# Kernel optimization log

Measured on AMD Instinct MI355X. Metric: run time of the kernel, lower is better.

## Reference

```python
import jax, jax.numpy as jnp
import numpy as np

D_MODEL = 1024
NUM_HEADS = 16
D_K = D_MODEL // NUM_HEADS
B, T = 2, 2048


def setup_inputs() -> dict:
    key = jax.random.key(0)
    ks = jax.random.split(key, 9)
    s = 1.0 / np.sqrt(D_MODEL)
    inp = {"x": jax.random.normal(ks[0], (B, T, D_MODEL), dtype=jnp.float32)}
    for i, name in enumerate(["q", "k", "v", "out"]):
        inp[f"W_{name}"] = jax.random.uniform(ks[1 + 2 * i], (D_MODEL, D_MODEL), jnp.float32, -s, s)
        inp[f"b_{name}"] = jax.random.uniform(ks[2 + 2 * i], (D_MODEL,), jnp.float32, -s, s)
    return inp


def reference(x, W_q, b_q, W_k, b_k, W_v, b_v, W_out, b_out):
    b, t, _ = x.shape
    # torch Linear: y = x @ W.T + b
    def proj(inp, W, bias):
        y = inp @ W.T + bias
        return y.reshape(b, -1, NUM_HEADS, D_K).transpose(0, 2, 1, 3)  # [B,H,T,d_k]

    Q = proj(x, W_q, b_q)
    K = proj(x, W_k, b_k)
    V = proj(x, W_v, b_v)
    scores = jnp.einsum("bhqd,bhkd->bhqk", Q, K) / jnp.sqrt(jnp.float32(D_K))
    attn = jax.nn.softmax(scores, axis=-1)
    ctx = jnp.einsum("bhqk,bhkd->bhqd", attn, V)
    ctx = ctx.transpose(0, 2, 1, 3).reshape(b, t, D_MODEL)
    return ctx @ W_out.T + b_out
```

## Files before the change

### kernel.cpp

```cpp
#include <hip/hip_runtime.h>
#include <hip/hip_bf16.h>

typedef __attribute__((ext_vector_type(8))) short short8;
typedef __attribute__((ext_vector_type(4))) short short4v;
typedef __attribute__((ext_vector_type(4))) float floatx4;

__device__ __forceinline__ unsigned short f2b(float f) {
  unsigned int v;
  __builtin_memcpy(&v, &f, 4);
  unsigned int r = (v + 0x7FFFu + ((v >> 16) & 1u)) >> 16;
  return (unsigned short)r;
}

__device__ __forceinline__ unsigned int f2b_pk(float a, float b) {
#if __has_builtin(__builtin_amdgcn_cvt_pk_bf16_f32)
  typedef __attribute__((ext_vector_type(2))) __bf16 bf16x2;
  bf16x2 r = __builtin_amdgcn_cvt_pk_bf16_f32(a, b);
  unsigned int u;
  __builtin_memcpy(&u, &r, 4);
  return u;
#else
  return ((unsigned int)f2b(b) << 16) | (unsigned int)f2b(a);
#endif
}

__device__ __forceinline__ float fast_exp2(float x) {
#if __has_builtin(__builtin_amdgcn_exp2f)
  return __builtin_amdgcn_exp2f(x);
#else
  return __builtin_exp2f(x);
#endif
}

__device__ __forceinline__ void async_copy16(const void* g, void* l) {
  __builtin_amdgcn_global_load_lds(
      (const __attribute__((address_space(1))) unsigned int*)g,
      (__attribute__((address_space(3))) unsigned int*)l, 16, 0, 0);
}

#define QSCALE 0.18033688011112042f


__global__ __launch_bounds__(256) void cvt_all_kernel(
    const float* __restrict__ x,
    const float* __restrict__ w0, const float* __restrict__ w1,
    const float* __restrict__ w2, const float* __restrict__ w3,
    unsigned short* __restrict__ xb,
    unsigned short* __restrict__ d0, unsigned short* __restrict__ d1,
    unsigned short* __restrict__ d2, unsigned short* __restrict__ d3)
{
  int gid = blockIdx.x * 256 + threadIdx.x;
  const float* src;
  unsigned short* dst;
  size_t off;
  if (gid < (1 << 20)) {
    src = x; dst = xb; off = gid;
  } else {
    int g = gid - (1 << 20);
    int w = g >> 18;
    off = g & 0x3FFFF;
    src = (w == 0) ? w0 : (w == 1) ? w1 : (w == 2) ? w2 : w3;
    dst = (w == 0) ? d0 : (w == 1) ? d1 : (w == 2) ? d2 : d3;
  }
  floatx4 v = *(const floatx4*)(src + off * 4);
  unsigned int lo = f2b_pk(v[0], v[1]), hi = f2b_pk(v[2], v[3]);
  unsigned long long r = ((unsigned long long)hi << 32) | lo;
  *(unsigned long long*)(dst + off * 4) = r;
}

__global__ __launch_bounds__(256) void gemm_qkv_kernel(
    const unsigned short* __restrict__ A,
    const unsigned short* __restrict__ W0, const unsigned short* __restrict__ W1,
    const unsigned short* __restrict__ W2,
    const float* __restrict__ bias0, const float* __restrict__ bias1,
    const float* __restrict__ bias2,
    unsigned short* __restrict__ Qo, unsigned short* __restrict__ Ko,
    unsigned short* __restrict__ VTo)
{
  const int z = blockIdx.z;
  const unsigned short* W  = (z == 0) ? W0 : (z == 1) ? W1 : W2;
  const float* bias        = (z == 0) ? bias0 : (z == 1) ? bias1 : bias2;

  __shared__ alignas(16) unsigned short sA[128 * 32];
  __shared__ alignas(16) unsigned short sB[128 * 32];

  const int tid  = threadIdx.x;
  const int lane = tid & 63;
  const int wave = tid >> 6;
  const int col  = lane & 15;
  const int quad = lane >> 4;
  const int wm   = (wave >> 1) * 64;
  const int wn   = (wave & 1) * 64;
  const int m0   = blockIdx.y * 128;
  const int n0   = blockIdx.x * 128;
  const int swz8 = (quad ^ ((col >> 1) & 3)) * 8;

  floatx4 acc[4][4];
#pragma unroll
  for (int i = 0; i < 4; ++i)
#pragma unroll
    for (int j = 0; j < 4; ++j) acc[i][j] = (floatx4){0.f, 0.f, 0.f, 0.f};

  for (int k0 = 0; k0 < 1024; k0 += 32) {
    __syncthreads();
#pragma unroll
    for (int i = 0; i < 2; ++i) {
      int c   = i * 256 + tid;
      int row = c >> 2;
      int cs  = (c & 3) ^ ((c >> 3) & 3);
      int ko  = cs * 8;
      async_copy16(A + (size_t)(m0 + row) * 1024 + k0 + ko, sA + c * 8);
      async_copy16(W + (size_t)(n0 + row) * 1024 + k0 + ko, sB + c * 8);
    }
    __syncthreads();
    short8 af[4], bf[4];
#pragma unroll
    for (int mi = 0; mi < 4; ++mi)
      af[mi] = *(const short8*)(sA + (wm + mi * 16 + col) * 32 + swz8);
#pragma unroll
    for (int ni = 0; ni < 4; ++ni)
      bf[ni] = *(const short8*)(sB + (wn + ni * 16 + col) * 32 + swz8);
#pragma unroll
    for (int mi = 0; mi < 4; ++mi)
#pragma unroll
      for (int ni = 0; ni < 4; ++ni)
        acc[mi][ni] = __builtin_amdgcn_mfma_f32_16x16x32_bf16(af[mi], bf[ni], acc[mi][ni], 0, 0, 0);
  }

#pragma unroll
  for (int ni = 0; ni < 4; ++ni) {
    int n = n0 + wn + ni * 16 + col;
    float bv = bias[n];
#pragma unroll
    for (int mi = 0; mi < 4; ++mi) {
      int mbase = m0 + wm + mi * 16 + quad * 4;
#pragma unroll
      for (int r = 0; r < 4; ++r) {
        int m = mbase + r;
        float val = acc[mi][ni][r] + bv;
        if (z == 0) {
          Qo[(size_t)m * 1024 + n] = f2b(val * QSCALE);
        } else if (z == 1) {
          Ko[(size_t)m * 1024 + n] = f2b(val);
        } else {
          int d = n & 63, h = n >> 6;
          int bb = m >> 11, t = m & 2047;
          VTo[(((size_t)bb * 16 + h) * 64 + d) * 2048 + t] = f2b(val);
        }
      }
    }
  }
}

__global__ __launch_bounds__(256) void gemm_out_kernel(
    const unsigned short* __restrict__ A, const unsigned short* __restrict__ W,
    const float* __restrict__ bias, float* __restrict__ DF)
{
  __shared__ alignas(16) unsigned short sA[128 * 32];
  __shared__ alignas(16) unsigned short sB[64 * 32];

  const int tid  = threadIdx.x;
  const int lane = tid & 63;
  const int wave = tid >> 6;
  const int col  = lane & 15;
  const int quad = lane >> 4;
  const int wm   = (wave >> 1) * 64;
  const int wn   = (wave & 1) * 32;
  const int m0   = blockIdx.y * 128;
  const int n0   = blockIdx.x * 64;
  const int swz8 = (quad ^ ((col >> 1) & 3)) * 8;

  floatx4 acc[4][2];
#pragma unroll
  for (int i = 0; i < 4; ++i)
#pragma unroll
    for (int j = 0; j < 2; ++j) acc[i][j] = (floatx4){0.f, 0.f, 0.f, 0.f};

  for (int k0 = 0; k0 < 1024; k0 += 32) {
    __syncthreads();
#pragma unroll
    for (int i = 0; i < 2; ++i) {
      int c   = i * 256 + tid;
      int row = c >> 2;
      int cs  = (c & 3) ^ ((c >> 3) & 3);
      async_copy16(A + (size_t)(m0 + row) * 1024 + k0 + cs * 8, sA + c * 8);
    }
    {
      int row = tid >> 2;
      int cs  = (tid & 3) ^ ((tid >> 3) & 3);
      async_copy16(W + (size_t)(n0 + row) * 1024 + k0 + cs * 8, sB + tid * 8);
    }
    __syncthreads();
    short8 af[4], bf[2];
#pragma unroll
    for (int mi = 0; mi < 4; ++mi)
      af[mi] = *(const short8*)(sA + (wm + mi * 16 + col) * 32 + swz8);
#pragma unroll
    for (int ni = 0; ni < 2; ++ni)
      bf[ni] = *(const short8*)(sB + (wn + ni * 16 + col) * 32 + swz8);
#pragma unroll
    for (int mi = 0; mi < 4; ++mi)
#pragma unroll
      for (int ni = 0; ni < 2; ++ni)
        acc[mi][ni] = __builtin_amdgcn_mfma_f32_16x16x32_bf16(af[mi], bf[ni], acc[mi][ni], 0, 0, 0);
  }

#pragma unroll
  for (int ni = 0; ni < 2; ++ni) {
    int n = n0 + wn + ni * 16 + col;
    float bv = bias[n];
#pragma unroll
    for (int mi = 0; mi < 4; ++mi) {
      int mbase = m0 + wm + mi * 16 + quad * 4;
#pragma unroll
      for (int r = 0; r < 4; ++r)
        DF[(size_t)(mbase + r) * 1024 + n] = acc[mi][ni][r] + bv;
    }
  }
}

__global__ __launch_bounds__(256, 6) void attention_kernel(
    const unsigned short* __restrict__ Q, const unsigned short* __restrict__ K,
    const unsigned short* __restrict__ VT, unsigned short* __restrict__ CTX)
{
  __shared__ alignas(16) unsigned short sQ[2 * 64 * 32];
  __shared__ alignas(16) unsigned short sK[2 * 64 * 32];
  __shared__ alignas(16) unsigned short sV[2 * 64 * 32];

  const int bh = blockIdx.x;
  const int b = bh >> 4, h = bh & 15;
  const int q0 = blockIdx.y * 64;
  const int tid  = threadIdx.x;
  const int lane = tid & 63;
  const int wave = tid >> 6;
  const int col  = lane & 15;
  const int quad = lane >> 4;
  const int swz8 = (quad ^ ((col >> 1) & 3)) * 8;

  const int srow = tid >> 2;
  const int sko  = ((tid & 3) ^ ((tid >> 3) & 3)) * 8;

#pragma unroll
  for (int i = 0; i < 2; ++i) {
    async_copy16(Q + (size_t)(b * 2048 + q0 + srow) * 1024 + h * 64 + i * 32 + sko,
                 sQ + (i * 256 + tid) * 8);
  }
  __syncthreads();
  short8 qf[2];
  qf[0] = *(const short8*)(sQ + (wave * 16 + col) * 32 + swz8);
  qf[1] = *(const short8*)(sQ + 2048 + (wave * 16 + col) * 32 + swz8);

  const int vsw  = (col >> 1) & 3;
  const int vch0 = ((quad >> 1) ^ vsw) * 8 + (quad & 1) * 4;
  const int vch1 = (((quad >> 1) | 2) ^ vsw) * 8 + (quad & 1) * 4;

  floatx4 Oacc[4];
#pragma unroll
  for (int nd = 0; nd < 4; ++nd) Oacc[nd] = (floatx4){0.f, 0.f, 0.f, 0.f};
  float lacc = 0.f;

  for (int kt = 0; kt < 2048; kt += 64) {
    __syncthreads();
#pragma unroll
    for (int i = 0; i < 2; ++i) {
      async_copy16(K + (size_t)(b * 2048 + kt + srow) * 1024 + h * 64 + i * 32 + sko,
                   sK + (i * 256 + tid) * 8);
      async_copy16(VT + ((size_t)bh * 64 + srow) * 2048 + kt + i * 32 + sko,
                   sV + (i * 256 + tid) * 8);
    }
    __syncthreads();

    floatx4 ST[4];
#pragma unroll
    for (int f = 0; f < 4; ++f) {
      ST[f] = (floatx4){0.f, 0.f, 0.f, 0.f};
      short8 kf0 = *(const short8*)(sK + (f * 16 + col) * 32 + swz8);
      ST[f] = __builtin_amdgcn_mfma_f32_16x16x32_bf16(kf0, qf[0], ST[f], 0, 0, 0);
      short8 kf1 = *(const short8*)(sK + 2048 + (f * 16 + col) * 32 + swz8);
      ST[f] = __builtin_amdgcn_mfma_f32_16x16x32_bf16(kf1, qf[1], ST[f], 0, 0, 0);
    }

    short8 pf[2];
#pragma unroll
    for (int s = 0; s < 2; ++s) {
      float p00 = fast_exp2(ST[2 * s][0]);
      float p01 = fast_exp2(ST[2 * s][1]);
      float p02 = fast_exp2(ST[2 * s][2]);
      float p03 = fast_exp2(ST[2 * s][3]);
      float p10 = fast_exp2(ST[2 * s + 1][0]);
      float p11 = fast_exp2(ST[2 * s + 1][1]);
      float p12 = fast_exp2(ST[2 * s + 1][2]);
      float p13 = fast_exp2(ST[2 * s + 1][3]);
      lacc += ((p00 + p01) + (p02 + p03)) + ((p10 + p11) + (p12 + p13));
      alignas(16) unsigned int d4[4] = {
          f2b_pk(p00, p01), f2b_pk(p02, p03), f2b_pk(p10, p11), f2b_pk(p12, p13)};
      __builtin_memcpy(&pf[s], d4, 16);
    }

#pragma unroll
    for (int s = 0; s < 2; ++s) {
#pragma unroll
      for (int nd = 0; nd < 4; ++nd) {
        const unsigned short* vrow = sV + s * 2048 + (nd * 16 + col) * 32;
        short4v v0 = *(const short4v*)(vrow + vch0);
        short4v v1 = *(const short4v*)(vrow + vch1);
        short8 vf = (short8){v0[0], v0[1], v0[2], v0[3], v1[0], v1[1], v1[2], v1[3]};
        Oacc[nd] = __builtin_amdgcn_mfma_f32_16x16x32_bf16(vf, pf[s], Oacc[nd], 0, 0, 0);
      }
    }
  }

  lacc += __shfl_xor(lacc, 16, 64);
  lacc += __shfl_xor(lacc, 32, 64);
  float inv = 1.f / lacc;

  {
    int q = q0 + wave * 16 + col;
    unsigned short* dst = CTX + (size_t)(b * 2048 + q) * 1024 + h * 64;
#pragma unroll
    for (int nd = 0; nd < 4; ++nd) {
      unsigned int lo = f2b_pk(Oacc[nd][0] * inv, Oacc[nd][1] * inv);
      unsigned int hi = f2b_pk(Oacc[nd][2] * inv, Oacc[nd][3] * inv);
      unsigned long long w = ((unsigned long long)hi << 32) | lo;
      *(unsigned long long*)(dst + nd * 16 + quad * 4) = w;
    }
  }
}

extern "C" void kernel_launch(void* const* d_in, const int* in_sizes, int n_in,
                              void* d_out, int out_size, void* d_ws, size_t ws_size,
                              hipStream_t stream) {
  const float* x   = (const float*)d_in[0];
  const float* W_q = (const float*)d_in[1];
  const float* b_q = (const float*)d_in[2];
  const float* W_k = (const float*)d_in[3];
  const float* b_k = (const float*)d_in[4];
  const float* W_v = (const float*)d_in[5];
  const float* b_v = (const float*)d_in[6];
  const float* W_o = (const float*)d_in[7];
  const float* b_o = (const float*)d_in[8];
  float* out = (float*)d_out;

  const size_t NX = (size_t)4096 * 1024;
  const size_t NW = (size_t)1024 * 1024;

  unsigned short* p   = (unsigned short*)d_ws;
  unsigned short* xb  = p;  p += NX;
  unsigned short* Wqb = p;  p += NW;
  unsigned short* Wkb = p;  p += NW;
  unsigned short* Wvb = p;  p += NW;
  unsigned short* Wob = p;  p += NW;
  unsigned short* Q   = p;  p += NX;
  unsigned short* Kb  = p;  p += NX;
  unsigned short* VT  = p;  p += NX;
  unsigned short* CTX = p;  p += NX;

  dim3 blk(256);
  cvt_all_kernel<<<dim3(8192), blk, 0, stream>>>(
      x, W_q, W_k, W_v, W_o, xb, Wqb, Wkb, Wvb, Wob);
  gemm_qkv_kernel<<<dim3(8, 32, 3), blk, 0, stream>>>(
      xb, Wqb, Wkb, Wvb, b_q, b_k, b_v, Q, Kb, VT);
  attention_kernel<<<dim3(32, 32), blk, 0, stream>>>(Q, Kb, VT, CTX);
  gemm_out_kernel<<<dim3(16, 32), blk, 0, stream>>>(CTX, Wob, b_o, out);
}
```

Before: 204.9 us.

## Pre-permute V^T layout in projection and compute softmax row sums via MFMA

The V projection epilogue now writes V^T with tokens permuted within each 32-wide chunk, packing four bf16 values into one 64-bit store. This lets the attention kernel load each V fragment with a single 16-byte LDS read instead of two 8-byte reads plus a shuffle. The softmax denominator is now accumulated with an extra MFMA against a ones vector instead of per-lane adds and cross-lane shuffles. The row sum is then built from bf16-rounded probabilities, which slightly changes numerics.

```diff
diff --git a/kernel.cpp b/kernel.cpp
--- a/kernel.cpp
+++ b/kernel.cpp
@@ -2,7 +2,6 @@
 #include <hip/hip_bf16.h>
 
 typedef __attribute__((ext_vector_type(8))) short short8;
-typedef __attribute__((ext_vector_type(4))) short short4v;
 typedef __attribute__((ext_vector_type(4))) float floatx4;
 
 __device__ __forceinline__ unsigned short f2b(float f) {
@@ -134,18 +133,22 @@
 #pragma unroll
     for (int mi = 0; mi < 4; ++mi) {
       int mbase = m0 + wm + mi * 16 + quad * 4;
-#pragma unroll
-      for (int r = 0; r < 4; ++r) {
-        int m = mbase + r;
-        float val = acc[mi][ni][r] + bv;
-        if (z == 0) {
-          Qo[(size_t)m * 1024 + n] = f2b(val * QSCALE);
-        } else if (z == 1) {
-          Ko[(size_t)m * 1024 + n] = f2b(val);
-        } else {
-          int d = n & 63, h = n >> 6;
-          int bb = m >> 11, t = m & 2047;
-          VTo[(((size_t)bb * 16 + h) * 64 + d) * 2048 + t] = f2b(val);
+      if (z == 2) {
+        int d = n & 63, hh = n >> 6;
+        int bb = mbase >> 11, tb = mbase & 2047;
+        int tl = tb & 31, tbase = tb & ~31;
+        int pp = ((tl & 15) >> 2) * 8 + ((tl >> 4) & 1) * 4;
+        unsigned int lo = f2b_pk(acc[mi][ni][0] + bv, acc[mi][ni][1] + bv);
+        unsigned int hi = f2b_pk(acc[mi][ni][2] + bv, acc[mi][ni][3] + bv);
+        unsigned long long w = ((unsigned long long)hi << 32) | lo;
+        *(unsigned long long*)(VTo + (((size_t)bb * 16 + hh) * 64 + d) * 2048 + tbase + pp) = w;
+      } else {
+#pragma unroll
+        for (int r = 0; r < 4; ++r) {
+          int m = mbase + r;
+          float val = acc[mi][ni][r] + bv;
+          if (z == 0) Qo[(size_t)m * 1024 + n] = f2b(val * QSCALE);
+          else        Ko[(size_t)m * 1024 + n] = f2b(val);
         }
       }
     }
@@ -250,14 +253,18 @@
   qf[0] = *(const short8*)(sQ + (wave * 16 + col) * 32 + swz8);
   qf[1] = *(const short8*)(sQ + 2048 + (wave * 16 + col) * 32 + swz8);
 
-  const int vsw  = (col >> 1) & 3;
-  const int vch0 = ((quad >> 1) ^ vsw) * 8 + (quad & 1) * 4;
-  const int vch1 = (((quad >> 1) | 2) ^ vsw) * 8 + (quad & 1) * 4;
+  short8 ones;
+  {
+    unsigned short o = 0x3F80;
+    short tmp[8] = {(short)o, (short)o, (short)o, (short)o,
+                    (short)o, (short)o, (short)o, (short)o};
+    __builtin_memcpy(&ones, tmp, 16);
+  }
 
   floatx4 Oacc[4];
 #pragma unroll
   for (int nd = 0; nd < 4; ++nd) Oacc[nd] = (floatx4){0.f, 0.f, 0.f, 0.f};
-  float lacc = 0.f;
+  floatx4 Osum = (floatx4){0.f, 0.f, 0.f, 0.f};
 
   for (int kt = 0; kt < 2048; kt += 64) {
     __syncthreads();
@@ -291,7 +298,6 @@
       float p11 = fast_exp2(ST[2 * s + 1][1]);
       float p12 = fast_exp2(ST[2 * s + 1][2]);
       float p13 = fast_exp2(ST[2 * s + 1][3]);
-      lacc += ((p00 + p01) + (p02 + p03)) + ((p10 + p11) + (p12 + p13));
       alignas(16) unsigned int d4[4] = {
           f2b_pk(p00, p01), f2b_pk(p02, p03), f2b_pk(p10, p11), f2b_pk(p12, p13)};
       __builtin_memcpy(&pf[s], d4, 16);
@@ -299,20 +305,16 @@
 
 #pragma unroll
     for (int s = 0; s < 2; ++s) {
+      Osum = __builtin_amdgcn_mfma_f32_16x16x32_bf16(ones, pf[s], Osum, 0, 0, 0);
 #pragma unroll
       for (int nd = 0; nd < 4; ++nd) {
-        const unsigned short* vrow = sV + s * 2048 + (nd * 16 + col) * 32;
-        short4v v0 = *(const short4v*)(vrow + vch0);
-        short4v v1 = *(const short4v*)(vrow + vch1);
-        short8 vf = (short8){v0[0], v0[1], v0[2], v0[3], v1[0], v1[1], v1[2], v1[3]};
+        short8 vf = *(const short8*)(sV + s * 2048 + (nd * 16 + col) * 32 + swz8);
         Oacc[nd] = __builtin_amdgcn_mfma_f32_16x16x32_bf16(vf, pf[s], Oacc[nd], 0, 0, 0);
       }
     }
   }
 
-  lacc += __shfl_xor(lacc, 16, 64);
-  lacc += __shfl_xor(lacc, 32, 64);
-  float inv = 1.f / lacc;
+  float inv = 1.f / Osum[0];
 
   {
     int q = q0 + wave * 16 + col;
```

Measured after the change: 211.8 us. 1.03x slower.
